# Kernel optimization log

Hardware: AMD Instinct MI355X
Metric: run time of the kernel (lower is better)

## Reference

```python
import jax, jax.numpy as jnp
import numpy as np

T, V, D = 8, 100000, 128   # tables, rows per table, embedding dim
B = 4096                   # batch (bags per table)
N = 204800                 # total jagged values per table (avg pooling factor 50)


def setup_inputs() -> dict:
    key = jax.random.key(0)
    k1, k2, k3, k4 = jax.random.split(key, 4)
    tables = jax.random.normal(k1, (T, V, D), dtype=jnp.float32) * 0.01
    values = jax.random.randint(k2, (T, N), 0, V, dtype=jnp.int32)
    # offsets per table: [0, sorted interior points, N]  (include_last_offset=True)
    interior = jnp.sort(jax.random.randint(k3, (T, B - 1), 0, N, dtype=jnp.int32), axis=1)
    zeros = jnp.zeros((T, 1), dtype=jnp.int32)
    ends = jnp.full((T, 1), N, dtype=jnp.int32)
    offsets = jnp.concatenate([zeros, interior, ends], axis=1)  # [T, B+1]
    per_sample_weights = jax.random.uniform(k4, (T, N), dtype=jnp.float32)
    return {"tables": tables, "values": values, "offsets": offsets,
            "per_sample_weights": per_sample_weights}


def reference(tables, values, offsets, per_sample_weights):
    # One EmbeddingBag(mode='sum', include_last_offset=True) per table, vmapped.
    n = values.shape[1]

    def one_table(w, vals, offs, psw):
        emb = w[vals] * psw[:, None]                      # [N, D] weighted gather
        # segment id of position i: j s.t. offs[j] <= i < offs[j+1]
        seg = jnp.searchsorted(offs, jnp.arange(n, dtype=offs.dtype), side='right') - 1
        return jax.ops.segment_sum(emb, seg, num_segments=B)  # [B, D]

    pooled = jax.vmap(one_table)(tables, values, offsets, per_sample_weights)  # [T, B, D]
    # concat per-table pooled embeddings along feature dim -> [B, T*D]
    return jnp.transpose(pooled, (1, 0, 2)).reshape(B, T * D)
```

## Files before the change

### kernel.cpp

```cpp
#include <hip/hip_runtime.h>


namespace {
constexpr int T = 8;
constexpr int V = 100000;
constexpr int D = 128;
constexpr int B = 4096;
constexpr int N = 204800;
}

__device__ __forceinline__ float readlane_f(float v, int l) {
    return __int_as_float(__builtin_amdgcn_readlane(__float_as_int(v), l));
}

__global__ __launch_bounds__(256) void grouped_ebag_kernel(
    const float* __restrict__ tables,
    const int* __restrict__ values,
    const int* __restrict__ offsets,
    const float* __restrict__ psw,
    float* __restrict__ out)
{
    const int wave = threadIdx.x >> 6;
    const int lane = threadIdx.x & 63;
    const int bag  = (blockIdx.x << 2) + wave;
    const int t = bag >> 12;
    const int b = bag & (B - 1);

    int start = offsets[t * (B + 1) + b];
    int end   = offsets[t * (B + 1) + b + 1];
    start = __builtin_amdgcn_readfirstlane(start);
    end   = __builtin_amdgcn_readfirstlane(end);
    const int len = end - start;

    const float* __restrict__ tab  = tables + (size_t)t * (V * D);
    const int*   __restrict__ vals = values + (size_t)t * N + start;
    const float* __restrict__ wgt  = psw    + (size_t)t * N + start;

    float2 acc = make_float2(0.f, 0.f);

    for (int base = 0; base < len; base += 64) {
        const int rem = len - base;
        const int m   = rem < 64 ? rem : 64;

        const int pos  = base + lane;
        const int posc = pos < len ? pos : (len - 1);
        const int   vidx = vals[posc];
        const float vw   = (pos < len) ? wgt[posc] : 0.f;

        const int ngrp = (m + 7) >> 3;

        float2 bufA[8], bufB[8];

        auto LOAD = [&](float2 (&buf)[8], int g) {
#pragma unroll
            for (int j = 0; j < 8; ++j) {
                const int r   = (g << 3) + j;
                const int row = __builtin_amdgcn_readlane(vidx, r);
                buf[j] = *(const float2*)(tab + (size_t)row * D + lane * 2);
            }
        };
        auto FMA = [&](float2 (&buf)[8], int g) {
#pragma unroll
            for (int j = 0; j < 8; ++j) {
                const int r = (g << 3) + j;
                const float w = readlane_f(vw, r);
                acc.x = fmaf(buf[j].x, w, acc.x);
                acc.y = fmaf(buf[j].y, w, acc.y);
            }
        };

        LOAD(bufA, 0);
        int g = 0;
        for (; g + 2 <= ngrp; g += 2) {
            LOAD(bufB, g + 1);
            FMA(bufA, g);
            if (g + 2 < ngrp) LOAD(bufA, g + 2);
            FMA(bufB, g + 1);
        }
        if (g < ngrp) FMA(bufA, g);
    }

    *(float2*)(out + (size_t)b * (T * D) + t * D + lane * 2) = acc;
}

extern "C" void kernel_launch(void* const* d_in, const int* in_sizes, int n_in,
                              void* d_out, int out_size, void* d_ws, size_t ws_size,
                              hipStream_t stream) {
    const float* tables  = (const float*)d_in[0];
    const int*   values  = (const int*)d_in[1];
    const int*   offsets = (const int*)d_in[2];
    const float* psw     = (const float*)d_in[3];
    float*       out     = (float*)d_out;

    dim3 grid((T * B) / 4);
    dim3 block(256);
    grouped_ebag_kernel<<<grid, block, 0, stream>>>(tables, values, offsets, psw, out);
}
```

Measured before the change: 565.8 us.

## Split gather per table and pre-stream each table into last-level cache

The single grouped gather launch is replaced by a loop over tables. For each table, a streaming kernel first reads the whole table sequentially with float4 loads, then a per-table gather kernel runs. The aim is to turn random 512-byte row fetches from HBM into hits in the large on-die cache by warming it with cheap sequential bandwidth. In exchange it reads every table in full once more and adds 16 kernel launches, and the benefit depends on the table fitting in cache and staying there.

```diff
diff --git a/kernel.cpp b/kernel.cpp
--- a/kernel.cpp
+++ b/kernel.cpp
@@ -7,24 +7,39 @@
 constexpr int D = 128;
 constexpr int B = 4096;
 constexpr int N = 204800;
+constexpr int PRE_BLOCKS = 1024;
+constexpr int F4_PER_TABLE = V * D / 4;
+constexpr int F4_PER_BLOCK = F4_PER_TABLE / PRE_BLOCKS;
 }
 
 __device__ __forceinline__ float readlane_f(float v, int l) {
     return __int_as_float(__builtin_amdgcn_readlane(__float_as_int(v), l));
 }
 
-__global__ __launch_bounds__(256) void grouped_ebag_kernel(
+__global__ __launch_bounds__(256) void prestream_kernel(
+    const float* __restrict__ tab)
+{
+    const float4* __restrict__ tp = (const float4*)tab;
+    const size_t base0 = (size_t)blockIdx.x * F4_PER_BLOCK;
+    float keep = 0.f;
+    for (int k = (int)threadIdx.x; k < F4_PER_BLOCK; k += 256) {
+        const float4 v4 = tp[base0 + k];
+        keep += v4.x + v4.y + v4.z + v4.w;
+    }
+    asm volatile("" :: "v"(keep));
+}
+
+__global__ __launch_bounds__(256) void gather_kernel(
     const float* __restrict__ tables,
     const int* __restrict__ values,
     const int* __restrict__ offsets,
     const float* __restrict__ psw,
-    float* __restrict__ out)
+    float* __restrict__ out,
+    int t)
 {
     const int wave = threadIdx.x >> 6;
     const int lane = threadIdx.x & 63;
-    const int bag  = (blockIdx.x << 2) + wave;
-    const int t = bag >> 12;
-    const int b = bag & (B - 1);
+    const int b    = (blockIdx.x << 2) + wave;
 
     int start = offsets[t * (B + 1) + b];
     int end   = offsets[t * (B + 1) + b + 1];
@@ -92,7 +107,10 @@
     const float* psw     = (const float*)d_in[3];
     float*       out     = (float*)d_out;
 
-    dim3 grid((T * B) / 4);
-    dim3 block(256);
-    grouped_ebag_kernel<<<grid, block, 0, stream>>>(tables, values, offsets, psw, out);
+    for (int t = 0; t < T; ++t) {
+        prestream_kernel<<<dim3(PRE_BLOCKS), dim3(256), 0, stream>>>(
+            tables + (size_t)t * (V * D));
+        gather_kernel<<<dim3(B / 4), dim3(256), 0, stream>>>(
+            tables, values, offsets, psw, out, t);
+    }
 }
```

Result: slower. 799.3 us (+41.3%).
